# Optimization experiments

Measured on AMD Instinct MI355X. Metric: run time of the kernel, lower is better.

## Reference

```python
import jax, jax.numpy as jnp
import numpy as np

ALPHA = 1.5      # entmax alpha (q parameter)
N_ITER = 50      # entmax-bisect iterations (entmax library default)
B, S, DM, H, HKV, HD = 1, 2048, 2048, 16, 4, 128
ROPE_THETA = 10000.0


def _entmax_p(x):
    """alpha-entmax along last axis via bisection on tau (matches entmax.EntmaxBisect)."""
    am1 = ALPHA - 1.0
    pw = 1.0 / am1
    X = x * am1
    d = x.shape[-1]
    max_val = jnp.max(X, axis=-1, keepdims=True)
    tau_lo = max_val - 1.0                      # _gp(1, alpha) = 1
    tau_hi = max_val - (1.0 / d) ** am1          # _gp(1/d, alpha)
    dm0 = tau_hi - tau_lo

    def body(i, carry):
        tau_lo, dm, tau_m = carry
        dm = dm * 0.5
        tau_m = tau_lo + dm
        p = jnp.maximum(X - tau_m, 0.0) ** pw
        f = jnp.sum(p, axis=-1, keepdims=True) - 1.0
        tau_lo = jnp.where(f >= 0, tau_m, tau_lo)
        return (tau_lo, dm, tau_m)

    tau_lo, dm, tau_m = jax.lax.fori_loop(0, N_ITER, body, (tau_lo, dm0, tau_lo))
    p = jnp.maximum(X - tau_m, 0.0) ** pw
    return p / jnp.sum(p, axis=-1, keepdims=True)  # ensure_sum_one


@jax.custom_vjp
def entmax_bisect(x):
    return _entmax_p(x)

def _emx_fwd(x):
    p = _entmax_p(x)
    return p, p

def _emx_bwd(p, g):
    # entmax library backward: gppr = p^(2-alpha) on support
    gppr = jnp.where(p > 0, p ** (2.0 - ALPHA), 0.0)
    dX = g * gppr
    q = jnp.sum(dX, axis=-1, keepdims=True) / jnp.sum(gppr, axis=-1, keepdims=True)
    return ((dX - q * gppr),)

entmax_bisect.defvjp(_emx_fwd, _emx_bwd)


def _rotate_half(x):
    x1, x2 = x[..., : HD // 2], x[..., HD // 2:]
    return jnp.concatenate([-x2, x1], axis=-1)


def setup_inputs() -> dict:
    key = jax.random.key(0)
    k1, k2, k3, k4, k5 = jax.random.split(key, 5)
    hidden_states = jax.random.normal(k1, (B, S, DM), dtype=jnp.float32)
    wq = jax.random.normal(k2, (H * HD, DM), dtype=jnp.float32) * 0.02
    wk = jax.random.normal(k3, (HKV * HD, DM), dtype=jnp.float32) * 0.02
    wv = jax.random.normal(k4, (HKV * HD, DM), dtype=jnp.float32) * 0.02
    wo = jax.random.normal(k5, (DM, H * HD), dtype=jnp.float32) * 0.02
    # real Llama RoPE position embeddings
    inv_freq = 1.0 / (ROPE_THETA ** (np.arange(0, HD, 2, dtype=np.float32) / HD))
    pos = np.arange(S, dtype=np.float32)
    freqs = pos[:, None] * inv_freq[None, :]          # [S, HD/2]
    emb = np.concatenate([freqs, freqs], axis=-1)     # [S, HD]
    cos = jnp.asarray(np.cos(emb))[None]              # [1, S, HD]
    sin = jnp.asarray(np.sin(emb))[None]
    return {"hidden_states": hidden_states, "cos": cos, "sin": sin,
            "wq": wq, "wk": wk, "wv": wv, "wo": wo}


def reference(hidden_states, cos, sin, wq, wk, wv, wo):
    b, s, _ = hidden_states.shape
    scaling = HD ** -0.5
    # QKV projections -> [B, H, S, HD]
    q = (hidden_states @ wq.T).reshape(b, s, H, HD).transpose(0, 2, 1, 3)
    k = (hidden_states @ wk.T).reshape(b, s, HKV, HD).transpose(0, 2, 1, 3)
    v = (hidden_states @ wv.T).reshape(b, s, HKV, HD).transpose(0, 2, 1, 3)
    # RoPE (cos/sin broadcast over head axis)
    c, sn = cos[:, None, :, :], sin[:, None, :, :]
    q = q * c + _rotate_half(q) * sn
    k = k * c + _rotate_half(k) * sn
    # GQA: repeat kv heads
    g = H // HKV
    k = jnp.repeat(k, g, axis=1)
    v = jnp.repeat(v, g, axis=1)
    scores = jnp.einsum('bhqd,bhkd->bhqk', q, k) * scaling
    causal = jnp.tril(jnp.ones((s, s), dtype=bool))
    scores = jnp.where(causal, scores, -jnp.inf)
    attn = entmax_bisect(scores)                      # [B, H, S, S]
    out = jnp.einsum('bhqk,bhkd->bhqd', attn, v)
    out = out.transpose(0, 2, 1, 3).reshape(b, s, H * HD)
    out = out @ wo.T
    return (out, attn)
```

## Files before the change

kernel.cpp:

```cpp
#include <hip/hip_runtime.h>

typedef __bf16 bf16;
typedef __bf16 bf16x4 __attribute__((ext_vector_type(4)));
typedef __bf16 bf16x8 __attribute__((ext_vector_type(8)));
typedef float f32x4 __attribute__((ext_vector_type(4)));
typedef float f32x2 __attribute__((ext_vector_type(2)));

#define S 2048
#define DM 2048
#define HD 128
#define H 16
#define NQKV 3072
#define NEWTON_ITERS 12
#define BROW 556

__device__ __forceinline__ void gl2lds16(const void* g, void* l) {
    __builtin_amdgcn_global_load_lds(
        (const __attribute__((address_space(1))) void*)g,
        (__attribute__((address_space(3))) void*)l, 16, 0, 0);
}

__device__ __forceinline__ void nt_store4(f32x4 v, float* p) {
    __builtin_nontemporal_store(v, (f32x4*)p);
}

template <int CTRL, int RM>
__device__ __forceinline__ float dpp_zero(float x) {
    return __builtin_bit_cast(float, __builtin_amdgcn_update_dpp(
        0, __builtin_bit_cast(int, x), CTRL, RM, 0xf, false));
}
template <int CTRL, int RM>
__device__ __forceinline__ float dpp_self(float x) {
    int xi = __builtin_bit_cast(int, x);
    return __builtin_bit_cast(float, __builtin_amdgcn_update_dpp(xi, xi, CTRL, RM, 0xf, false));
}
__device__ __forceinline__ float wave_bcast63(float x) {
    return __builtin_bit_cast(float, __builtin_amdgcn_readlane(__builtin_bit_cast(int, x), 63));
}
__device__ __forceinline__ float wave_sum(float x) {
    x += dpp_zero<0x111, 0xf>(x);
    x += dpp_zero<0x112, 0xf>(x);
    x += dpp_zero<0x114, 0xf>(x);
    x += dpp_zero<0x118, 0xf>(x);
    x += dpp_zero<0x142, 0xa>(x);
    x += dpp_zero<0x143, 0xc>(x);
    return wave_bcast63(x);
}
__device__ __forceinline__ float wave_fmax(float x) {
    x = fmaxf(x, dpp_self<0x111, 0xf>(x));
    x = fmaxf(x, dpp_self<0x112, 0xf>(x));
    x = fmaxf(x, dpp_self<0x114, 0xf>(x));
    x = fmaxf(x, dpp_self<0x118, 0xf>(x));
    x = fmaxf(x, dpp_self<0x142, 0xa>(x));
    x = fmaxf(x, dpp_self<0x143, 0xc>(x));
    return wave_bcast63(x);
}

__global__ void cvt_all(const float* __restrict__ hid, const float* __restrict__ wq,
                        const float* __restrict__ wk, const float* __restrict__ wv,
                        const float* __restrict__ wo, bf16* __restrict__ bh,
                        bf16* __restrict__ bqkv, bf16* __restrict__ bwo) {
    int i = blockIdx.x * blockDim.x + threadIdx.x;
    const float* src;
    bf16* dst;
    int off;
    if (i < 1048576) { src = hid; dst = bh; off = i; }
    else if (i < 2097152) { src = wq; dst = bqkv; off = i - 1048576; }
    else if (i < 2359296) { src = wk; dst = bqkv + 2048 * 2048; off = i - 2097152; }
    else if (i < 2621440) { src = wv; dst = bqkv + 2048 * 2048 + 512 * 2048; off = i - 2359296; }
    else { src = wo; dst = bwo; off = i - 2621440; }
    float4 f = ((const float4*)src)[off];
    bf16x4 o;
    o[0] = (bf16)f.x; o[1] = (bf16)f.y; o[2] = (bf16)f.z; o[3] = (bf16)f.w;
    ((bf16x4*)dst)[off] = o;
}

template <int BM, int BN>
__global__ __launch_bounds__(256) void gemm_bt(const bf16* __restrict__ A,
                                               const bf16* __restrict__ B,
                                               float* __restrict__ C, int Ndim, int K) {
    __shared__ bf16 As[BM * 32];
    __shared__ bf16 Bs[BN * 32];
    int m0 = blockIdx.x * BM, n0 = blockIdx.y * BN;
    int t = threadIdx.x;
    int l = t & 63, w = t >> 6;
    int lane16 = l & 15, quad = l >> 4;

    const bf16* Abase = A + (size_t)m0 * K;
    const bf16* Bbase = B + (size_t)n0 * K;

    constexpr int MI = BM / 32, NI = BN / 32;
    int wm = (w & 1) * (BM / 2), wn = (w >> 1) * (BN / 2);
    f32x4 acc[MI][NI];
#pragma unroll
    for (int i = 0; i < MI; i++)
#pragma unroll
        for (int j = 0; j < NI; j++) acc[i][j] = (f32x4){0.f, 0.f, 0.f, 0.f};

    constexpr int AG = BM * 4;
    constexpr int BG = BN * 4;

    for (int k0 = 0; k0 < K; k0 += 32) {
#pragma unroll
        for (int it = 0; it < AG / 256; it++) {
            int c = it * 256 + t;
            gl2lds16(Abase + (size_t)(c >> 2) * K + k0 + (c & 3) * 8, &As[(c - l) * 8]);
        }
#pragma unroll
        for (int it = 0; it < BG / 256; it++) {
            int c = it * 256 + t;
            gl2lds16(Bbase + (size_t)(c >> 2) * K + k0 + (c & 3) * 8, &Bs[(c - l) * 8]);
        }
        __syncthreads();
        bf16x8 af[MI], bfr[NI];
#pragma unroll
        for (int i = 0; i < MI; i++)
            af[i] = *(const bf16x8*)&As[(wm + i * 16 + lane16) * 32 + quad * 8];
#pragma unroll
        for (int j = 0; j < NI; j++)
            bfr[j] = *(const bf16x8*)&Bs[(wn + j * 16 + lane16) * 32 + quad * 8];
#pragma unroll
        for (int i = 0; i < MI; i++)
#pragma unroll
            for (int j = 0; j < NI; j++)
                acc[i][j] = __builtin_amdgcn_mfma_f32_16x16x32_bf16(af[i], bfr[j], acc[i][j], 0, 0, 0);
        __syncthreads();
    }
#pragma unroll
    for (int i = 0; i < MI; i++)
#pragma unroll
        for (int j = 0; j < NI; j++) {
            float* cp = C + (size_t)(m0 + wm + i * 16 + quad * 4) * Ndim + n0 + wn + j * 16 + lane16;
#pragma unroll
            for (int r = 0; r < 4; r++) cp[(size_t)r * Ndim] = acc[i][j][r];
        }
}

__global__ void rope_qk(const float* __restrict__ qkv, const float* __restrict__ cosb,
                        const float* __restrict__ sinb, bf16* __restrict__ qs,
                        bf16* __restrict__ kb) {
    int col = blockIdx.x * 256 + threadIdx.x;
    int s = blockIdx.y;
    const float* row = qkv + (size_t)s * NQKV;
    float v = row[col];
    if (col < DM) {
        int h = col >> 7, d = col & 127;
        float c = cosb[s * HD + d], sn = sinb[s * HD + d];
        float other = row[(h << 7) + ((d < 64) ? (d + 64) : (d - 64))];
        float rot = (d < 64) ? -other : other;
        float o = v * c + rot * sn;
        qs[((size_t)h * S + s) * HD + d] = (bf16)(o * 0.04419417382415922f);
    } else {
        int c2 = col - DM;
        int kv = c2 >> 7, d = c2 & 127;
        float c = cosb[s * HD + d], sn = sinb[s * HD + d];
        float other = row[DM + (kv << 7) + ((d < 64) ? (d + 64) : (d - 64))];
        float rot = (d < 64) ? -other : other;
        float o = v * c + rot * sn;
        kb[((size_t)kv * S + s) * HD + d] = (bf16)o;
    }
}

__global__ __launch_bounds__(256) void vtrans(const float* __restrict__ qkv, bf16* __restrict__ vT) {
    __shared__ bf16 tile[64][66];
    int s0 = blockIdx.x * 64, y0 = blockIdx.y * 64;
    int t = threadIdx.x;
    int ty = t & 63, tr = t >> 6;
#pragma unroll
    for (int i = 0; i < 16; i++) {
        int s = tr + i * 4;
        float v = qkv[(size_t)(s0 + s) * NQKV + 2560 + y0 + ty];
        tile[s][ty] = (bf16)v;
    }
    __syncthreads();
#pragma unroll
    for (int i = 0; i < 16; i++) {
        int y = tr + i * 4;
        vT[(size_t)(y0 + y) * S + s0 + ty] = tile[ty][y];
    }
}

template <int SEGS>
__device__ __forceinline__ void attn_body(const bf16* __restrict__ qs, const bf16* __restrict__ kb,
                                          const bf16* __restrict__ vT, float* __restrict__ attn,
                                          bf16* __restrict__ o, int r0, int h,
                                          float (&buf)[16][BROW]) {
    constexpr int NREG2 = SEGS * 4;
    int jlen = r0 + 16;
    int l = threadIdx.x & 63;
    int w = threadIdx.x >> 6;
    int lane16 = l & 15, quad = l >> 4;

    const bf16* qrow = qs + ((size_t)h * S + (r0 + lane16)) * HD + quad * 8;
    bf16x8 afrag[4];
#pragma unroll
    for (int kc = 0; kc < 4; kc++) afrag[kc] = *(const bf16x8*)(qrow + kc * 32);

    const bf16* kbase = kb + (size_t)(h >> 2) * S * HD;
    const bf16* vbase = vT + (size_t)(h >> 2) * HD * S;
    f32x2 xr[NREG2];

#pragma unroll
    for (int sgi = 0; sgi < SEGS; sgi++) {
        int j0 = sgi * 512;
        float (*sb)[BROW] = buf;
#pragma unroll
        for (int tt = 0; tt < 2; tt++) {
            int t = w + tt * 16;
            int jt = j0 + t * 16;
            if (jt < jlen) {
                f32x4 acc = {0.f, 0.f, 0.f, 0.f};
                const bf16* kp = kbase + (size_t)(jt + lane16) * HD + quad * 8;
#pragma unroll
                for (int kc = 0; kc < 4; kc++) {
                    bf16x8 b = *(const bf16x8*)(kp + kc * 32);
                    acc = __builtin_amdgcn_mfma_f32_16x16x32_bf16(afrag[kc], b, acc, 0, 0, 0);
                }
                if (jt + 15 > r0) {
                    int jj = jt + lane16;
#pragma unroll
                    for (int r = 0; r < 4; r++) {
                        int rowi = quad * 4 + r;
                        float v = acc[r];
                        if (jj > r0 + rowi) v = -1e30f;
                        sb[rowi][t * 16 + lane16] = v;
                    }
                } else {
#pragma unroll
                    for (int r = 0; r < 4; r++) sb[quad * 4 + r][t * 16 + lane16] = acc[r];
                }
            }
        }
        __syncthreads();
#pragma unroll
        for (int part = 0; part < 2; part++) {
            float4 fq = *(const float4*)&sb[w][part * 256 + l * 4];
            if (sgi == SEGS - 1) {
                int jb = j0 + part * 256 + l * 4;
                xr[sgi * 4 + part * 2 + 0] =
                    (f32x2){(jb + 0 < jlen) ? fq.x : -1e30f, (jb + 1 < jlen) ? fq.y : -1e30f};
                xr[sgi * 4 + part * 2 + 1] =
                    (f32x2){(jb + 2 < jlen) ? fq.z : -1e30f, (jb + 3 < jlen) ? fq.w : -1e30f};
            } else {
                xr[sgi * 4 + part * 2 + 0] = (f32x2){fq.x, fq.y};
                xr[sgi * 4 + part * 2 + 1] = (f32x2){fq.z, fq.w};
            }
        }
        __syncthreads();
    }

    const f32x2 z2 = {0.f, 0.f};
    float mx = -1e30f;
#pragma unroll
    for (int c = 0; c < NREG2; c++) mx = fmaxf(mx, fmaxf(xr[c][0], xr[c][1]));
    float m = wave_fmax(mx);

    float tau = m - 1.0f;
#pragma unroll 1
    for (int it = 0; it < NEWTON_ITERS; it++) {
        f32x2 tvi = {tau, tau};
        f32x2 fa = z2, fb = z2, ga = z2, gb = z2;
#pragma unroll
        for (int c = 0; c < NREG2; c += 2) {
            f32x2 t0 = __builtin_elementwise_max(xr[c] - tvi, z2);
            fa += t0 * t0; ga += t0;
            f32x2 t1 = __builtin_elementwise_max(xr[c + 1] - tvi, z2);
            fb += t1 * t1; gb += t1;
        }
        f32x2 fv = fa + fb, gv = ga + gb;
        float f = wave_sum(fv[0] + fv[1]);
        float g = wave_sum(gv[0] + gv[1]);
        tau += (f - 1.0f) / (2.0f * g + 1e-20f);
    }

    f32x2 tv = {tau, tau};
    float inv;
    {
        f32x2 sa = z2, sbv = z2;
#pragma unroll
        for (int c = 0; c < NREG2; c += 2) {
            f32x2 t0 = __builtin_elementwise_max(xr[c] - tv, z2);
            sa += t0 * t0;
            f32x2 t1 = __builtin_elementwise_max(xr[c + 1] - tv, z2);
            sbv += t1 * t1;
        }
        f32x2 sv = sa + sbv;
        float ssum = wave_sum(sv[0] + sv[1]);
        inv = 1.0f / ssum;
    }

    int jt_o = (w & 7) * 16;
    int kh = (w >> 3) * 256;
    f32x4 acc_o = {0.f, 0.f, 0.f, 0.f};
    f32x2 inv2 = {inv, inv};

#pragma unroll
    for (int sgi = 0; sgi < SEGS; sgi++) {
        int j0 = sgi * 512;
        bf16 (*pb)[BROW] = (bf16(*)[BROW])(&buf[0][0]) + (sgi & 1) * 16;
#pragma unroll
        for (int part = 0; part < 2; part++) {
            f32x2 ta = __builtin_elementwise_max(xr[sgi * 4 + part * 2 + 0] - tv, z2);
            f32x2 tb = __builtin_elementwise_max(xr[sgi * 4 + part * 2 + 1] - tv, z2);
            f32x2 pa = (ta * ta) * inv2;
            f32x2 pb2 = (tb * tb) * inv2;
            bf16x4 pbv;
            pbv[0] = (bf16)pa[0]; pbv[1] = (bf16)pa[1];
            pbv[2] = (bf16)pb2[0]; pbv[3] = (bf16)pb2[1];
            *(bf16x4*)&pb[w][part * 256 + l * 4] = pbv;
        }
        __syncthreads();
#pragma unroll
        for (int ks = 0; ks < 8; ks++) {
            int kk = kh + ks * 32;
            bf16x8 a = *(const bf16x8*)&pb[lane16][kk + quad * 8];
            bf16x8 b = *(const bf16x8*)(vbase + (size_t)(jt_o + lane16) * S + j0 + kk + quad * 8);
            acc_o = __builtin_amdgcn_mfma_f32_16x16x32_bf16(a, b, acc_o, 0, 0, 0);
        }
    }

    __syncthreads();
    if (w >= 8) {
#pragma unroll
        for (int r = 0; r < 4; r++) buf[w - 8][l * 4 + r] = acc_o[r];
    }
    __syncthreads();
    if (w < 8) {
        bf16* op = o + (size_t)(r0 + quad * 4) * DM + h * HD + jt_o + lane16;
#pragma unroll
        for (int r = 0; r < 4; r++) {
            float v = acc_o[r] + buf[w][l * 4 + r];
            op[(size_t)r * DM] = (bf16)v;
        }
    }

    float* arow = attn + ((size_t)h * S + (r0 + w)) * S;
#pragma unroll
    for (int sgi = 0; sgi < SEGS; sgi++) {
        int j0 = sgi * 512;
#pragma unroll
        for (int part = 0; part < 2; part++) {
            f32x2 ta = __builtin_elementwise_max(xr[sgi * 4 + part * 2 + 0] - tv, z2);
            f32x2 tb = __builtin_elementwise_max(xr[sgi * 4 + part * 2 + 1] - tv, z2);
            f32x2 pa = (ta * ta) * inv2;
            f32x2 pb2 = (tb * tb) * inv2;
            f32x4 pv = {pa[0], pa[1], pb2[0], pb2[1]};
            nt_store4(pv, &arow[j0 + part * 256 + l * 4]);
        }
    }
    f32x4 z4 = {0.f, 0.f, 0.f, 0.f};
    for (int j = SEGS * 512 + l * 4; j < S; j += 256) nt_store4(z4, &arow[j]);
}

__global__ __attribute__((amdgpu_flat_work_group_size(1024, 1024), amdgpu_waves_per_eu(8)))
void attn_av_all(const bf16* __restrict__ qs,
                 const bf16* __restrict__ kb,
                 const bf16* __restrict__ vT,
                 float* __restrict__ attn,
                 bf16* __restrict__ o) {
    __shared__ float buf[16][BROW];
    int b = blockIdx.x;
    int h = b & 15;
    int qh = b >> 4;
    attn_body<4>(qs, kb, vT, attn, o, (96 + qh) * 16, h, buf);
    __syncthreads();
    attn_body<3>(qs, kb, vT, attn, o, (64 + qh) * 16, h, buf);
    __syncthreads();
    attn_body<2>(qs, kb, vT, attn, o, (32 + qh) * 16, h, buf);
    __syncthreads();
    attn_body<1>(qs, kb, vT, attn, o, qh * 16, h, buf);
}

extern "C" void kernel_launch(void* const* d_in, const int* in_sizes, int n_in,
                              void* d_out, int out_size, void* d_ws, size_t ws_size,
                              hipStream_t stream) {
    const float* hidden = (const float*)d_in[0];
    const float* cosb   = (const float*)d_in[1];
    const float* sinb   = (const float*)d_in[2];
    const float* wq     = (const float*)d_in[3];
    const float* wk     = (const float*)d_in[4];
    const float* wv     = (const float*)d_in[5];
    const float* wo     = (const float*)d_in[6];
    char* ws = (char*)d_ws;
    bf16*  bf_hidden = (bf16*)(ws);
    bf16*  bf_wqkv   = (bf16*)(ws + 8388608);
    bf16*  bf_wo     = (bf16*)(ws + 20971520);
    float* qkv_raw   = (float*)(ws + 29360128);
    bf16*  qsb       = (bf16*)(ws + 54525952);
    bf16*  kbb       = (bf16*)(ws + 62914560);
    bf16*  vTb       = (bf16*)(ws + 65011712);
    float* out  = (float*)d_out;
    float* attn = out + 4194304;

    cvt_all<<<dim3(14336), 256, 0, stream>>>(hidden, wq, wk, wv, wo, bf_hidden, bf_wqkv, bf_wo);

    gemm_bt<64, 128><<<dim3(32, 24), 256, 0, stream>>>(bf_hidden, bf_wqkv, qkv_raw, NQKV, DM);

    rope_qk<<<dim3(10, S), 256, 0, stream>>>(qkv_raw, cosb, sinb, qsb, kbb);
    vtrans<<<dim3(32, 8), 256, 0, stream>>>(qkv_raw, vTb);

    attn_av_all<<<dim3(512), 1024, 0, stream>>>(qsb, kbb, vTb, attn, bf_hidden);

    gemm_bt<64, 128><<<dim3(32, 16), 256, 0, stream>>>(bf_hidden, bf_wo, out, DM, DM);
}
```

Baseline: 601.4 us.

## Halve attention block size, store scores in fp16 registers, rebalance causal work

Result: faster. 585.5 us (-2.6%).

```diff
diff --git a/kernel.cpp b/kernel.cpp
--- a/kernel.cpp
+++ b/kernel.cpp
@@ -5,6 +5,7 @@
 typedef __bf16 bf16x8 __attribute__((ext_vector_type(8)));
 typedef float f32x4 __attribute__((ext_vector_type(4)));
 typedef float f32x2 __attribute__((ext_vector_type(2)));
+typedef _Float16 f16x2 __attribute__((ext_vector_type(2)));
 
 #define S 2048
 #define DM 2048
@@ -13,6 +14,7 @@
 #define NQKV 3072
 #define NEWTON_ITERS 12
 #define BROW 556
+#define MASKV -30000.0f
 
 __device__ __forceinline__ void gl2lds16(const void* g, void* l) {
     __builtin_amdgcn_global_load_lds(
@@ -185,7 +187,7 @@
                                           const bf16* __restrict__ vT, float* __restrict__ attn,
                                           bf16* __restrict__ o, int r0, int h,
                                           float (&buf)[16][BROW]) {
-    constexpr int NREG2 = SEGS * 4;
+    constexpr int NR = SEGS * 4;
     int jlen = r0 + 16;
     int l = threadIdx.x & 63;
     int w = threadIdx.x >> 6;
@@ -198,101 +200,115 @@
 
     const bf16* kbase = kb + (size_t)(h >> 2) * S * HD;
     const bf16* vbase = vT + (size_t)(h >> 2) * HD * S;
-    f32x2 xr[NREG2];
+    f16x2 xr0[NR], xr1[NR];
 
 #pragma unroll
     for (int sgi = 0; sgi < SEGS; sgi++) {
         int j0 = sgi * 512;
-        float (*sb)[BROW] = buf;
-#pragma unroll
-        for (int tt = 0; tt < 2; tt++) {
-            int t = w + tt * 16;
-            int jt = j0 + t * 16;
+#pragma unroll
+        for (int tt = 0; tt < 4; tt++) {
+            int jt = j0 + (w + tt * 8) * 16;
             if (jt < jlen) {
                 f32x4 acc = {0.f, 0.f, 0.f, 0.f};
                 const bf16* kp = kbase + (size_t)(jt + lane16) * HD + quad * 8;
 #pragma unroll
                 for (int kc = 0; kc < 4; kc++) {
-                    bf16x8 b = *(const bf16x8*)(kp + kc * 32);
-                    acc = __builtin_amdgcn_mfma_f32_16x16x32_bf16(afrag[kc], b, acc, 0, 0, 0);
+                    bf16x8 bfr = *(const bf16x8*)(kp + kc * 32);
+                    acc = __builtin_amdgcn_mfma_f32_16x16x32_bf16(afrag[kc], bfr, acc, 0, 0, 0);
                 }
+                int tcol = (w + tt * 8) * 16 + lane16;
                 if (jt + 15 > r0) {
                     int jj = jt + lane16;
 #pragma unroll
                     for (int r = 0; r < 4; r++) {
                         int rowi = quad * 4 + r;
                         float v = acc[r];
-                        if (jj > r0 + rowi) v = -1e30f;
-                        sb[rowi][t * 16 + lane16] = v;
+                        if (jj > r0 + rowi) v = MASKV;
+                        buf[rowi][tcol] = v;
                     }
                 } else {
 #pragma unroll
-                    for (int r = 0; r < 4; r++) sb[quad * 4 + r][t * 16 + lane16] = acc[r];
+                    for (int r = 0; r < 4; r++) buf[quad * 4 + r][tcol] = acc[r];
                 }
             }
         }
         __syncthreads();
 #pragma unroll
         for (int part = 0; part < 2; part++) {
-            float4 fq = *(const float4*)&sb[w][part * 256 + l * 4];
+            float4 fq0 = *(const float4*)&buf[w][part * 256 + l * 4];
+            float4 fq1 = *(const float4*)&buf[w + 8][part * 256 + l * 4];
+            f32x2 a0, b0, a1, b1;
             if (sgi == SEGS - 1) {
                 int jb = j0 + part * 256 + l * 4;
-                xr[sgi * 4 + part * 2 + 0] =
-                    (f32x2){(jb + 0 < jlen) ? fq.x : -1e30f, (jb + 1 < jlen) ? fq.y : -1e30f};
-                xr[sgi * 4 + part * 2 + 1] =
-                    (f32x2){(jb + 2 < jlen) ? fq.z : -1e30f, (jb + 3 < jlen) ? fq.w : -1e30f};
+                bool c0 = jb + 0 < jlen, c1 = jb + 1 < jlen, c2 = jb + 2 < jlen, c3 = jb + 3 < jlen;
+                a0 = (f32x2){c0 ? fq0.x : MASKV, c1 ? fq0.y : MASKV};
+                b0 = (f32x2){c2 ? fq0.z : MASKV, c3 ? fq0.w : MASKV};
+                a1 = (f32x2){c0 ? fq1.x : MASKV, c1 ? fq1.y : MASKV};
+                b1 = (f32x2){c2 ? fq1.z : MASKV, c3 ? fq1.w : MASKV};
             } else {
-                xr[sgi * 4 + part * 2 + 0] = (f32x2){fq.x, fq.y};
-                xr[sgi * 4 + part * 2 + 1] = (f32x2){fq.z, fq.w};
+                a0 = (f32x2){fq0.x, fq0.y}; b0 = (f32x2){fq0.z, fq0.w};
+                a1 = (f32x2){fq1.x, fq1.y}; b1 = (f32x2){fq1.z, fq1.w};
             }
+            xr0[sgi * 4 + part * 2 + 0] = __builtin_convertvector(a0, f16x2);
+            xr0[sgi * 4 + part * 2 + 1] = __builtin_convertvector(b0, f16x2);
+            xr1[sgi * 4 + part * 2 + 0] = __builtin_convertvector(a1, f16x2);
+            xr1[sgi * 4 + part * 2 + 1] = __builtin_convertvector(b1, f16x2);
         }
         __syncthreads();
     }
 
     const f32x2 z2 = {0.f, 0.f};
-    float mx = -1e30f;
-#pragma unroll
-    for (int c = 0; c < NREG2; c++) mx = fmaxf(mx, fmaxf(xr[c][0], xr[c][1]));
-    float m = wave_fmax(mx);
-
-    float tau = m - 1.0f;
+    float mx0 = MASKV, mx1 = MASKV;
+#pragma unroll
+    for (int c = 0; c < NR; c++) {
+        f32x2 x0 = __builtin_convertvector(xr0[c], f32x2);
+        f32x2 x1 = __builtin_convertvector(xr1[c], f32x2);
+        mx0 = fmaxf(mx0, fmaxf(x0[0], x0[1]));
+        mx1 = fmaxf(mx1, fmaxf(x1[0], x1[1]));
+    }
+    float tau0 = wave_fmax(mx0) - 1.0f;
+    float tau1 = wave_fmax(mx1) - 1.0f;
 #pragma unroll 1
     for (int it = 0; it < NEWTON_ITERS; it++) {
-        f32x2 tvi = {tau, tau};
-        f32x2 fa = z2, fb = z2, ga = z2, gb = z2;
-#pragma unroll
-        for (int c = 0; c < NREG2; c += 2) {
-            f32x2 t0 = __builtin_elementwise_max(xr[c] - tvi, z2);
-            fa += t0 * t0; ga += t0;
-            f32x2 t1 = __builtin_elementwise_max(xr[c + 1] - tvi, z2);
-            fb += t1 * t1; gb += t1;
-        }
-        f32x2 fv = fa + fb, gv = ga + gb;
-        float f = wave_sum(fv[0] + fv[1]);
-        float g = wave_sum(gv[0] + gv[1]);
-        tau += (f - 1.0f) / (2.0f * g + 1e-20f);
-    }
-
-    f32x2 tv = {tau, tau};
-    float inv;
+        f32x2 tv0i = {tau0, tau0}, tv1i = {tau1, tau1};
+        f32x2 fa0 = z2, ga0 = z2, fa1 = z2, ga1 = z2;
+#pragma unroll
+        for (int c = 0; c < NR; c++) {
+            f32x2 x0 = __builtin_convertvector(xr0[c], f32x2);
+            f32x2 d0 = __builtin_elementwise_max(x0 - tv0i, z2);
+            fa0 += d0 * d0; ga0 += d0;
+            f32x2 x1 = __builtin_convertvector(xr1[c], f32x2);
+            f32x2 d1 = __builtin_elementwise_max(x1 - tv1i, z2);
+            fa1 += d1 * d1; ga1 += d1;
+        }
+        float f0 = wave_sum(fa0[0] + fa0[1]);
+        float g0 = wave_sum(ga0[0] + ga0[1]);
+        float f1 = wave_sum(fa1[0] + fa1[1]);
+        float g1 = wave_sum(ga1[0] + ga1[1]);
+        tau0 += (f0 - 1.0f) / (2.0f * g0 + 1e-20f);
+        tau1 += (f1 - 1.0f) / (2.0f * g1 + 1e-20f);
+    }
+
+    f32x2 tv0 = {tau0, tau0}, tv1 = {tau1, tau1};
+    float inv0, inv1;
     {
-        f32x2 sa = z2, sbv = z2;
-#pragma unroll
-        for (int c = 0; c < NREG2; c += 2) {
-            f32x2 t0 = __builtin_elementwise_max(xr[c] - tv, z2);
-            sa += t0 * t0;
-            f32x2 t1 = __builtin_elementwise_max(xr[c + 1] - tv, z2);
-            sbv += t1 * t1;
-        }
-        f32x2 sv = sa + sbv;
-        float ssum = wave_sum(sv[0] + sv[1]);
-        inv = 1.0f / ssum;
-    }
-
-    int jt_o = (w & 7) * 16;
-    int kh = (w >> 3) * 256;
+        f32x2 sa0 = z2, sa1 = z2;
+#pragma unroll
+        for (int c = 0; c < NR; c++) {
+            f32x2 x0 = __builtin_convertvector(xr0[c], f32x2);
+            f32x2 d0 = __builtin_elementwise_max(x0 - tv0, z2);
+            sa0 += d0 * d0;
+            f32x2 x1 = __builtin_convertvector(xr1[c], f32x2);
+            f32x2 d1 = __builtin_elementwise_max(x1 - tv1, z2);
+            sa1 += d1 * d1;
+        }
+        inv0 = 1.0f / wave_sum(sa0[0] + sa0[1]);
+        inv1 = 1.0f / wave_sum(sa1[0] + sa1[1]);
+    }
+
+    int jt_o = w * 16;
     f32x4 acc_o = {0.f, 0.f, 0.f, 0.f};
-    f32x2 inv2 = {inv, inv};
+    f32x2 i0 = {inv0, inv0}, i1 = {inv1, inv1};
 
 #pragma unroll
     for (int sgi = 0; sgi < SEGS; sgi++) {
@@ -300,59 +316,71 @@
         bf16 (*pb)[BROW] = (bf16(*)[BROW])(&buf[0][0]) + (sgi & 1) * 16;
 #pragma unroll
         for (int part = 0; part < 2; part++) {
-            f32x2 ta = __builtin_elementwise_max(xr[sgi * 4 + part * 2 + 0] - tv, z2);
-            f32x2 tb = __builtin_elementwise_max(xr[sgi * 4 + part * 2 + 1] - tv, z2);
-            f32x2 pa = (ta * ta) * inv2;
-            f32x2 pb2 = (tb * tb) * inv2;
-            bf16x4 pbv;
-            pbv[0] = (bf16)pa[0]; pbv[1] = (bf16)pa[1];
-            pbv[2] = (bf16)pb2[0]; pbv[3] = (bf16)pb2[1];
-            *(bf16x4*)&pb[w][part * 256 + l * 4] = pbv;
-        }
-        __syncthreads();
-#pragma unroll
-        for (int ks = 0; ks < 8; ks++) {
-            int kk = kh + ks * 32;
+            f32x2 xa = __builtin_convertvector(xr0[sgi * 4 + part * 2 + 0], f32x2);
+            f32x2 xb = __builtin_convertvector(xr0[sgi * 4 + part * 2 + 1], f32x2);
+            f32x2 da = __builtin_elementwise_max(xa - tv0, z2);
+            f32x2 db = __builtin_elementwise_max(xb - tv0, z2);
+            f32x2 pa = (da * da) * i0;
+            f32x2 pc = (db * db) * i0;
+            bf16x4 pv;
+            pv[0] = (bf16)pa[0]; pv[1] = (bf16)pa[1]; pv[2] = (bf16)pc[0]; pv[3] = (bf16)pc[1];
+            *(bf16x4*)&pb[w][part * 256 + l * 4] = pv;
+            xa = __builtin_convertvector(xr1[sgi * 4 + part * 2 + 0], f32x2);
+            xb = __builtin_convertvector(xr1[sgi * 4 + part * 2 + 1], f32x2);
+            da = __builtin_elementwise_max(xa - tv1, z2);
+            db = __builtin_elementwise_max(xb - tv1, z2);
+            pa = (da * da) * i1;
+            pc = (db * db) * i1;
+            pv[0] = (bf16)pa[0]; pv[1] = (bf16)pa[1]; pv[2] = (bf16)pc[0]; pv[3] = (bf16)pc[1];
+            *(bf16x4*)&pb[w + 8][part * 256 + l * 4] = pv;
+        }
+        __syncthreads();
+#pragma unroll
+        for (int ks = 0; ks < 16; ks++) {
+            int kk = ks * 32;
             bf16x8 a = *(const bf16x8*)&pb[lane16][kk + quad * 8];
-            bf16x8 b = *(const bf16x8*)(vbase + (size_t)(jt_o + lane16) * S + j0 + kk + quad * 8);
-            acc_o = __builtin_amdgcn_mfma_f32_16x16x32_bf16(a, b, acc_o, 0, 0, 0);
-        }
-    }
-
-    __syncthreads();
-    if (w >= 8) {
-#pragma unroll
-        for (int r = 0; r < 4; r++) buf[w - 8][l * 4 + r] = acc_o[r];
-    }
-    __syncthreads();
-    if (w < 8) {
-        bf16* op = o + (size_t)(r0 + quad * 4) * DM + h * HD + jt_o + lane16;
-#pragma unroll
-        for (int r = 0; r < 4; r++) {
-            float v = acc_o[r] + buf[w][l * 4 + r];
-            op[(size_t)r * DM] = (bf16)v;
-        }
-    }
-
-    float* arow = attn + ((size_t)h * S + (r0 + w)) * S;
+            bf16x8 bv = *(const bf16x8*)(vbase + (size_t)(jt_o + lane16) * S + j0 + kk + quad * 8);
+            acc_o = __builtin_amdgcn_mfma_f32_16x16x32_bf16(a, bv, acc_o, 0, 0, 0);
+        }
+    }
+
+    bf16* op = o + (size_t)(r0 + quad * 4) * DM + h * HD + jt_o + lane16;
+#pragma unroll
+    for (int r = 0; r < 4; r++) op[(size_t)r * DM] = (bf16)acc_o[r];
+
+    float* arow0 = attn + ((size_t)h * S + (r0 + w)) * S;
+    float* arow1 = arow0 + (size_t)8 * S;
 #pragma unroll
     for (int sgi = 0; sgi < SEGS; sgi++) {
         int j0 = sgi * 512;
 #pragma unroll
         for (int part = 0; part < 2; part++) {
-            f32x2 ta = __builtin_elementwise_max(xr[sgi * 4 + part * 2 + 0] - tv, z2);
-            f32x2 tb = __builtin_elementwise_max(xr[sgi * 4 + part * 2 + 1] - tv, z2);
-            f32x2 pa = (ta * ta) * inv2;
-            f32x2 pb2 = (tb * tb) * inv2;
-            f32x4 pv = {pa[0], pa[1], pb2[0], pb2[1]};
-            nt_store4(pv, &arow[j0 + part * 256 + l * 4]);
+            f32x2 xa = __builtin_convertvector(xr0[sgi * 4 + part * 2 + 0], f32x2);
+            f32x2 xb = __builtin_convertvector(xr0[sgi * 4 + part * 2 + 1], f32x2);
+            f32x2 da = __builtin_elementwise_max(xa - tv0, z2);
+            f32x2 db = __builtin_elementwise_max(xb - tv0, z2);
+            f32x2 pa = (da * da) * i0;
+            f32x2 pc = (db * db) * i0;
+            f32x4 pv0 = {pa[0], pa[1], pc[0], pc[1]};
+            nt_store4(pv0, &arow0[j0 + part * 256 + l * 4]);
+            xa = __builtin_convertvector(xr1[sgi * 4 + part * 2 + 0], f32x2);
+            xb = __builtin_convertvector(xr1[sgi * 4 + part * 2 + 1], f32x2);
+            da = __builtin_elementwise_max(xa - tv1, z2);
+            db = __builtin_elementwise_max(xb - tv1, z2);
+            pa = (da * da) * i1;
+            pc = (db * db) * i1;
+            f32x4 pv1 = {pa[0], pa[1], pc[0], pc[1]};
+            nt_store4(pv1, &arow1[j0 + part * 256 + l * 4]);
         }
     }
     f32x4 z4 = {0.f, 0.f, 0.f, 0.f};
-    for (int j = SEGS * 512 + l * 4; j < S; j += 256) nt_store4(z4, &arow[j]);
-}
-
-__global__ __attribute__((amdgpu_flat_work_group_size(1024, 1024), amdgpu_waves_per_eu(8)))
+    for (int j = SEGS * 512 + l * 4; j < S; j += 256) {
+        nt_store4(z4, &arow0[j]);
+        nt_store4(z4, &arow1[j]);
+    }
+}
+
+__global__ __attribute__((amdgpu_flat_work_group_size(512, 512), amdgpu_waves_per_eu(6)))
 void attn_av_all(const bf16* __restrict__ qs,
                  const bf16* __restrict__ kb,
                  const bf16* __restrict__ vT,
@@ -360,15 +388,22 @@
                  bf16* __restrict__ o) {
     __shared__ float buf[16][BROW];
     int b = blockIdx.x;
-    int h = b & 15;
-    int qh = b >> 4;
-    attn_body<4>(qs, kb, vT, attn, o, (96 + qh) * 16, h, buf);
-    __syncthreads();
-    attn_body<3>(qs, kb, vT, attn, o, (64 + qh) * 16, h, buf);
-    __syncthreads();
-    attn_body<2>(qs, kb, vT, attn, o, (32 + qh) * 16, h, buf);
-    __syncthreads();
-    attn_body<1>(qs, kb, vT, attn, o, qh * 16, h, buf);
+    if (b < 512) {
+        int h = b & 15;
+        int qh = b >> 4;
+        attn_body<4>(qs, kb, vT, attn, o, (96 + qh) * 16, h, buf);
+        __syncthreads();
+        attn_body<2>(qs, kb, vT, attn, o, (32 + qh) * 16, h, buf);
+        __syncthreads();
+        attn_body<1>(qs, kb, vT, attn, o, qh * 16, h, buf);
+    } else {
+        int b2 = b - 512;
+        int h = b2 & 15;
+        int q2 = b2 >> 4;
+        attn_body<3>(qs, kb, vT, attn, o, (64 + 2 * q2) * 16, h, buf);
+        __syncthreads();
+        attn_body<3>(qs, kb, vT, attn, o, (64 + 2 * q2 + 1) * 16, h, buf);
+    }
 }
 
 extern "C" void kernel_launch(void* const* d_in, const int* in_sizes, int n_in,
@@ -399,7 +434,7 @@
     rope_qk<<<dim3(10, S), 256, 0, stream>>>(qkv_raw, cosb, sinb, qsb, kbb);
     vtrans<<<dim3(32, 8), 256, 0, stream>>>(qkv_raw, vTb);
 
-    attn_av_all<<<dim3(512), 1024, 0, stream>>>(qsb, kbb, vTb, attn, bf_hidden);
+    attn_av_all<<<dim3(768), 512, 0, stream>>>(qsb, kbb, vTb, attn, bf_hidden);
 
     gemm_bt<64, 128><<<dim3(32, 16), 256, 0, stream>>>(bf_hidden, bf_wo, out, DM, DM);
 }
```
